# Performance work log

Hardware: AMD Instinct MI355X
Metric: run time of the kernel (lower is better)

## Reference

```python
import jax, jax.numpy as jnp
import numpy as np

S, B, D = 128, 32, 512
H = 512
L = 2
V = 8000


def _mk_lstm_params(key, in_dim, hid, layers):
    ks = jax.random.split(key, 4 * layers)
    s = 1.0 / np.sqrt(hid)
    W_ih = jnp.stack([jax.random.uniform(ks[4 * j + 0], (4 * hid, in_dim if j == 0 else hid), minval=-s, maxval=s) for j in range(layers)])
    W_hh = jnp.stack([jax.random.uniform(ks[4 * j + 1], (4 * hid, hid), minval=-s, maxval=s) for j in range(layers)])
    b_ih = jnp.stack([jax.random.uniform(ks[4 * j + 2], (4 * hid,), minval=-s, maxval=s) for j in range(layers)])
    b_hh = jnp.stack([jax.random.uniform(ks[4 * j + 3], (4 * hid,), minval=-s, maxval=s) for j in range(layers)])
    return W_ih, W_hh, b_ih, b_hh


def setup_inputs() -> dict:
    key = jax.random.key(0)
    kx, kf, kb, kwf, kwb = jax.random.split(key, 5)
    x = jax.random.normal(kx, (S, B, D), dtype=jnp.float32)
    Wf_ih, Wf_hh, bf_ih, bf_hh = _mk_lstm_params(kf, D, H, L)
    Wb_ih, Wb_hh, bb_ih, bb_hh = _mk_lstm_params(kb, D, H, L)
    s = 1.0 / np.sqrt(H)
    W_fwd = jax.random.uniform(kwf, (V, H), minval=-s, maxval=s)
    b_fwd = jnp.zeros((V,), jnp.float32)
    W_bwd = jax.random.uniform(kwb, (V, H), minval=-s, maxval=s)
    b_bwd = jnp.zeros((V,), jnp.float32)
    return {"x": x,
            "Wf_ih": Wf_ih, "Wf_hh": Wf_hh, "bf_ih": bf_ih, "bf_hh": bf_hh,
            "Wb_ih": Wb_ih, "Wb_hh": Wb_hh, "bb_ih": bb_ih, "bb_hh": bb_hh,
            "W_fwd": W_fwd, "b_fwd": b_fwd, "W_bwd": W_bwd, "b_bwd": b_bwd}


def _stacked_lstm(x_seq, W_ih, W_hh, b_ih, b_hh):
    """x_seq: [S,B,D]; params stacked over layers [L,4H,*]. Returns top-layer h over time: [S,B,H]."""
    layers = W_ih.shape[0]
    batch = x_seq.shape[1]
    h0 = jnp.zeros((layers, batch, H), x_seq.dtype)
    c0 = jnp.zeros((layers, batch, H), x_seq.dtype)

    def step(carry, x_t):
        h, c = carry
        hs, cs = [], []
        inp = x_t
        for j in range(layers):
            gates = inp @ W_ih[j].T + b_ih[j] + h[j] @ W_hh[j].T + b_hh[j]  # [B,4H]
            i_g, f_g, g_g, o_g = jnp.split(gates, 4, axis=-1)
            c_j = jax.nn.sigmoid(f_g) * c[j] + jax.nn.sigmoid(i_g) * jnp.tanh(g_g)
            h_j = jax.nn.sigmoid(o_g) * jnp.tanh(c_j)
            hs.append(h_j)
            cs.append(c_j)
            inp = h_j
        return (jnp.stack(hs), jnp.stack(cs)), inp

    _, out = jax.lax.scan(step, (h0, c0), x_seq)
    return out  # [S,B,H]


def reference(x, Wf_ih, Wf_hh, bf_ih, bf_hh, Wb_ih, Wb_hh, bb_ih, bb_hh, W_fwd, b_fwd, W_bwd, b_bwd):
    fwd_h = _stacked_lstm(x, Wf_ih, Wf_hh, bf_ih, bf_hh)                    # [S,B,H]
    bwd_h = _stacked_lstm(x[::-1], Wb_ih, Wb_hh, bb_ih, bb_hh)[::-1]        # [S,B,H]
    forward_dis = fwd_h @ W_fwd.T + b_fwd                                   # [S,B,V]
    backward_dis = bwd_h @ W_bwd.T + b_bwd                                  # [S,B,V]
    return (forward_dis, backward_dis)
```

## Files before the change

### kernel.cpp

```cpp
#include <hip/hip_runtime.h>

#define SS 128
#define BB 32
#define HH 512
#define VV 8000
#define VPAD 8064

typedef __bf16 bf16_t;
typedef __bf16 bf16x8 __attribute__((ext_vector_type(8)));
typedef float  floatx4 __attribute__((ext_vector_type(4)));
typedef unsigned int u32x4 __attribute__((ext_vector_type(4)));

__device__ __forceinline__ float sigmoidf_(float x) { return 1.0f / (1.0f + expf(-x)); }
__device__ __forceinline__ bf16x8 as_bf16x8(u32x4 v) { return __builtin_bit_cast(bf16x8, v); }

#define WS_FLG   0
#define WS_HHI   1024
#define WS_HLO   (WS_HHI + 524288)
#define WS_XHI   (WS_HLO + 524288)
#define WS_XLO   (WS_XHI + 4194304)
#define WS_HOUT  (WS_XLO + 4194304)
#define WS_WP    (WS_HOUT + 8388608)
#define MEMSET_BYTES WS_XHI

#define SMEM_BYTES 149632


__global__ __launch_bounds__(256)
void prep_x(const float* __restrict__ x, bf16_t* __restrict__ xh, bf16_t* __restrict__ xl) {
    int i = blockIdx.x * 256 + threadIdx.x;
    float v = x[i];
    bf16_t h = (bf16_t)v;
    xh[i] = h;
    xl[i] = (bf16_t)(v - (float)h);
}

__global__ __launch_bounds__(256)
void prep_wp(const float* __restrict__ Wf, const float* __restrict__ Wb, bf16_t* __restrict__ Wp) {
    int i = blockIdx.x * 256 + threadIdx.x;
    int k   = i & 511;
    int rd  = i >> 9;
    int row = rd % 8064;
    int d   = rd / 8064;
    const float* W = d ? Wb : Wf;
    Wp[i] = (row < VV) ? (bf16_t)W[(size_t)row * 512 + k] : (bf16_t)0.0f;
}


__global__ __launch_bounds__(512, 2)
void lstm_persist(const float* __restrict__ Wf_ih, const float* __restrict__ Wf_hh,
                  const float* __restrict__ Wb_ih, const float* __restrict__ Wb_hh,
                  const float* __restrict__ bf_ih, const float* __restrict__ bf_hh,
                  const float* __restrict__ bb_ih, const float* __restrict__ bb_hh,
                  const bf16_t* __restrict__ x_hi, const bf16_t* __restrict__ x_lo,
                  bf16_t* __restrict__ h_hi, bf16_t* __restrict__ h_lo,
                  bf16_t* __restrict__ hout, int* __restrict__ flg)
{
    extern __shared__ char smem[];
    bf16_t* wlds = (bf16_t*)smem;
    float*  pbuf = (float*)(smem + 131072);
    float*  bsum = (float*)(smem + 131072 + 18432);

    const int bid  = blockIdx.x;
    const int d    = bid >> 7;
    const int l    = (bid >> 6) & 1;
    const int s    = bid & 63;
    const int gid  = d * 2 + l;
    const int tid  = threadIdx.x;
    const int lane = tid & 63;
    const int kq   = tid >> 6;
    const int half = kq >> 2;
    const int kb   = kq & 3;
    const int lrow = lane & 15;
    const int quad = lane >> 4;

    const float* Wih = (d ? Wb_ih : Wf_ih) + (size_t)l * (2048 * 512);
    const float* Whh = (d ? Wb_hh : Wf_hh) + (size_t)l * (2048 * 512);

    if (tid < 32) {
        int g = tid >> 3, c = tid & 7;
        int grow = g * 512 + s * 8 + c;
        bsum[tid] = (d ? bb_ih : bf_ih)[l * 2048 + grow] + (d ? bb_hh : bf_hh)[l * 2048 + grow];
    }

    {
        const float* Wsrc = half ? Whh : Wih;
        bf16x8* w8 = (bf16x8*)wlds;
#pragma unroll
        for (int j = 0; j < 4; ++j)
#pragma unroll
            for (int nt = 0; nt < 2; ++nt) {
                int n    = nt * 16 + lrow;
                int grow = (n >> 3) * 512 + s * 8 + (n & 7);
                const float* src = Wsrc + (size_t)grow * 512 + (kb * 128 + j * 32 + quad * 8);
                bf16x8 vh, vl;
#pragma unroll
                for (int e = 0; e < 8; ++e) {
                    float v = src[e];
                    bf16_t hb = (bf16_t)v;
                    vh[e] = hb;
                    vl[e] = (bf16_t)(v - (float)hb);
                }
                int cidx = ((kq * 4 + j) * 2 + nt) * 2;
                w8[(size_t)cidx * 64 + lane]       = vh;
                w8[(size_t)(cidx + 1) * 64 + lane] = vl;
            }
    }
    __syncthreads();

    const bf16x8* wv8 = (const bf16x8*)wlds + (size_t)kq * 1024 + lane;
    const int aoff = lrow * 512 + kb * 128 + quad * 8;
    const bool xwave = (half == 0) && (l == 0);

    const int* wflag = nullptr;
    int  woff = 0;
    if (half == 1)      { wflag = flg + gid * 64;       woff = 0; }
    else if (l == 1)    { wflag = flg + (gid - 1) * 64; woff = 1; }

    float creg = 0.0f;

#pragma unroll 1
    for (int t = 0; t < SS; ++t) {
        const int slot_c = t & 3, slot_p = (t + 3) & 3;

        u32x4 rA0[4], rA1[4], rB0[4], rB1[4];

        if (wflag) {
            const int thr = t + woff;
            for (;;) {
                int v = __hip_atomic_load(wflag + lane, __ATOMIC_RELAXED, __HIP_MEMORY_SCOPE_AGENT);
                if (__all(v >= thr)) break;
                __builtin_amdgcn_s_sleep(2);
            }
        }

        if (xwave) {
            int t_x = d ? (SS - 1 - t) : t;
            const bf16_t* ah = x_hi + (size_t)t_x * 16384 + aoff;
            const bf16_t* al = x_lo + (size_t)t_x * 16384 + aoff;
#pragma unroll
            for (int j = 0; j < 4; ++j) {
                rA0[j] = *(const u32x4*)(ah + j * 32);
                rA1[j] = *(const u32x4*)(ah + 8192 + j * 32);
                rB0[j] = *(const u32x4*)(al + j * 32);
                rB1[j] = *(const u32x4*)(al + 8192 + j * 32);
            }
        } else {
            const bf16_t *pH, *pL;
            if (half == 0) {
                pH = h_hi + (size_t)((d * 2) * 4 + slot_c) * 16384;
                pL = h_lo + (size_t)((d * 2) * 4 + slot_c) * 16384;
            } else {
                pH = h_hi + (size_t)(gid * 4 + slot_p) * 16384;
                pL = h_lo + (size_t)(gid * 4 + slot_p) * 16384;
            }
            const bf16_t* ah  = pH + aoff;
            const bf16_t* ah2 = ah + 8192;
            const bf16_t* al  = pL + aoff;
            const bf16_t* al2 = al + 8192;
            asm volatile(
                "global_load_dwordx4 %0, %16, off sc1\n\t"
                "global_load_dwordx4 %4, %17, off sc1\n\t"
                "global_load_dwordx4 %8, %18, off sc1\n\t"
                "global_load_dwordx4 %12, %19, off sc1\n\t"
                "global_load_dwordx4 %1, %16, off offset:64 sc1\n\t"
                "global_load_dwordx4 %5, %17, off offset:64 sc1\n\t"
                "global_load_dwordx4 %9, %18, off offset:64 sc1\n\t"
                "global_load_dwordx4 %13, %19, off offset:64 sc1\n\t"
                "global_load_dwordx4 %2, %16, off offset:128 sc1\n\t"
                "global_load_dwordx4 %6, %17, off offset:128 sc1\n\t"
                "global_load_dwordx4 %10, %18, off offset:128 sc1\n\t"
                "global_load_dwordx4 %14, %19, off offset:128 sc1\n\t"
                "global_load_dwordx4 %3, %16, off offset:192 sc1\n\t"
                "global_load_dwordx4 %7, %17, off offset:192 sc1\n\t"
                "global_load_dwordx4 %11, %19, off offset:192 sc1\n\t"
                "global_load_dwordx4 %15, %19, off offset:192 sc1\n\t"
                "s_waitcnt vmcnt(8)"
                : "=&v"(rA0[0]), "=&v"(rA0[1]), "=&v"(rA0[2]), "=&v"(rA0[3]),
                  "=&v"(rA1[0]), "=&v"(rA1[1]), "=&v"(rA1[2]), "=&v"(rA1[3]),
                  "=&v"(rB0[0]), "=&v"(rB0[1]), "=&v"(rB0[2]), "=&v"(rB0[3]),
                  "=&v"(rB1[0]), "=&v"(rB1[1]), "=&v"(rB1[2]), "=&v"(rB1[3])
                : "v"(ah), "v"(ah2), "v"(al), "v"(al2)
                : "memory");
        }

        floatx4 acc00 = {0,0,0,0}, acc01 = {0,0,0,0}, acc10 = {0,0,0,0}, acc11 = {0,0,0,0};
#pragma unroll
        for (int j = 0; j < 4; ++j) {
            if (j == 2 && !xwave) {
                asm volatile("s_waitcnt vmcnt(0)"
                             : "+v"(rA0[2]), "+v"(rA0[3]), "+v"(rA1[2]), "+v"(rA1[3]),
                               "+v"(rB0[2]), "+v"(rB0[3]), "+v"(rB1[2]), "+v"(rB1[3]));
            }
            bf16x8 b0h = wv8[j * 256];
            bf16x8 b0l = wv8[j * 256 + 64];
            bf16x8 b1h = wv8[j * 256 + 128];
            bf16x8 b1l = wv8[j * 256 + 192];
            bf16x8 ah0 = as_bf16x8(rA0[j]);
            bf16x8 ah1 = as_bf16x8(rA1[j]);
            bf16x8 al0 = as_bf16x8(rB0[j]);
            bf16x8 al1 = as_bf16x8(rB1[j]);
            acc00 = __builtin_amdgcn_mfma_f32_16x16x32_bf16(ah0, b0h, acc00, 0, 0, 0);
            acc00 = __builtin_amdgcn_mfma_f32_16x16x32_bf16(ah0, b0l, acc00, 0, 0, 0);
            acc00 = __builtin_amdgcn_mfma_f32_16x16x32_bf16(al0, b0h, acc00, 0, 0, 0);
            acc01 = __builtin_amdgcn_mfma_f32_16x16x32_bf16(ah0, b1h, acc01, 0, 0, 0);
            acc01 = __builtin_amdgcn_mfma_f32_16x16x32_bf16(ah0, b1l, acc01, 0, 0, 0);
            acc01 = __builtin_amdgcn_mfma_f32_16x16x32_bf16(al0, b1h, acc01, 0, 0, 0);
            acc10 = __builtin_amdgcn_mfma_f32_16x16x32_bf16(ah1, b0h, acc10, 0, 0, 0);
            acc10 = __builtin_amdgcn_mfma_f32_16x16x32_bf16(ah1, b0l, acc10, 0, 0, 0);
            acc10 = __builtin_amdgcn_mfma_f32_16x16x32_bf16(al1, b0h, acc10, 0, 0, 0);
            acc11 = __builtin_amdgcn_mfma_f32_16x16x32_bf16(ah1, b1h, acc11, 0, 0, 0);
            acc11 = __builtin_amdgcn_mfma_f32_16x16x32_bf16(ah1, b1l, acc11, 0, 0, 0);
            acc11 = __builtin_amdgcn_mfma_f32_16x16x32_bf16(al1, b1h, acc11, 0, 0, 0);
        }

        if (half == 0) {
#pragma unroll
            for (int rg = 0; rg < 4; ++rg) {
                pbuf[kb * 1152 + (quad * 4 + rg) * 36 + lrow]           = acc00[rg];
                pbuf[kb * 1152 + (quad * 4 + rg) * 36 + 16 + lrow]      = acc01[rg];
                pbuf[kb * 1152 + (16 + quad * 4 + rg) * 36 + lrow]      = acc10[rg];
                pbuf[kb * 1152 + (16 + quad * 4 + rg) * 36 + 16 + lrow] = acc11[rg];
            }
        }
        __syncthreads();
        if (half == 1) {
#pragma unroll
            for (int rg = 0; rg < 4; ++rg) {
                pbuf[kb * 1152 + (quad * 4 + rg) * 36 + lrow]           += acc00[rg];
                pbuf[kb * 1152 + (quad * 4 + rg) * 36 + 16 + lrow]      += acc01[rg];
                pbuf[kb * 1152 + (16 + quad * 4 + rg) * 36 + lrow]      += acc10[rg];
                pbuf[kb * 1152 + (16 + quad * 4 + rg) * 36 + 16 + lrow] += acc11[rg];
            }
        }
        __syncthreads();

        bf16_t hh_keep = (bf16_t)0.0f;
        if (tid < 256) {
            if (l == 0 && t >= 4) {
                const int* gf = flg + (gid + 1) * 64;
                const int thr = t - 3;
                for (;;) {
                    int v = __hip_atomic_load(gf + lane, __ATOMIC_RELAXED, __HIP_MEMORY_SCOPE_AGENT);
                    if (__all(v >= thr)) break;
                    __builtin_amdgcn_s_sleep(2);
                }
            }
            int b = tid >> 3, c = tid & 7;
            float gi = 0.f, gf_ = 0.f, gg = 0.f, go = 0.f;
#pragma unroll
            for (int kbb = 0; kbb < 4; ++kbb) {
                int base = kbb * 1152 + b * 36 + c;
                gi  += pbuf[base];
                gf_ += pbuf[base + 8];
                gg  += pbuf[base + 16];
                go  += pbuf[base + 24];
            }
            gi += bsum[c]; gf_ += bsum[8 + c]; gg += bsum[16 + c]; go += bsum[24 + c];
            float cn = sigmoidf_(gf_) * creg + sigmoidf_(gi) * tanhf(gg);
            float hn = sigmoidf_(go) * tanhf(cn);
            creg = cn;
            bf16_t hh = (bf16_t)hn;
            bf16_t hl = (bf16_t)(hn - (float)hh);
            hh_keep = hh;
            int col = s * 8 + c;
            size_t ho = (size_t)(gid * 4 + slot_c) * 16384 + (size_t)b * HH + col;
            unsigned int vh = (unsigned int)__builtin_bit_cast(unsigned short, hh);
            unsigned int vl = (unsigned int)__builtin_bit_cast(unsigned short, hl);
            const bf16_t* ph = h_hi + ho;
            const bf16_t* pl = h_lo + ho;
            asm volatile(
                "global_store_short %0, %2, off sc1\n\t"
                "global_store_short %1, %3, off sc1\n\t"
                "s_waitcnt vmcnt(0)"
                :: "v"(ph), "v"(pl), "v"(vh), "v"(vl)
                : "memory");
        }

        __syncthreads();
        if (tid == 0) {
            __hip_atomic_store(flg + gid * 64 + s, t + 1,
                               __ATOMIC_RELAXED, __HIP_MEMORY_SCOPE_AGENT);
        }
        if (l == 1 && tid < 256) {
            int b = tid >> 3, c = tid & 7;
            int col = s * 8 + c;
            int t_x = d ? (SS - 1 - t) : t;
            hout[((size_t)(d * SS + t_x) * BB + b) * HH + col] = hh_keep;
        }
    }
}

__global__ __launch_bounds__(256)
void proj_gemm(const bf16_t* __restrict__ hA, const bf16_t* __restrict__ Wp,
               const float* __restrict__ b_fwd, const float* __restrict__ b_bwd,
               float* __restrict__ out)
{
    const int bid = blockIdx.x;
    const int nb  = (bid & 7) + ((bid >> 8) << 3);
    const int mb  = (bid >> 3) & 31;
    if (nb >= 63) return;
    const int d  = blockIdx.z;
    const int n0 = nb * 128;
    const int m0 = mb * 128;
    const bf16_t* A  = hA + (size_t)d * (SS * BB * HH);
    const bf16_t* Bw = Wp + (size_t)d * ((size_t)VPAD * HH);
    const float* bias = d ? b_bwd : b_fwd;
    float* O = out + (size_t)d * ((size_t)SS * BB * VV);

    __shared__ __align__(16) bf16_t lds_a[128 * 40];
    __shared__ __align__(16) bf16_t lds_b[128 * 40];

    const int tid  = threadIdx.x;
    const int lane = tid & 63;
    const int wv   = tid >> 6;
    const int wm   = wv >> 1, wn = wv & 1;
    const int lrow = lane & 15, quad = lane >> 4;

    floatx4 acc[4][4];
#pragma unroll
    for (int i = 0; i < 4; ++i)
#pragma unroll
        for (int j = 0; j < 4; ++j) acc[i][j] = (floatx4){0.f, 0.f, 0.f, 0.f};

    for (int k0 = 0; k0 < HH; k0 += 32) {
        __syncthreads();
#pragma unroll
        for (int q2 = 0; q2 < 2; ++q2) {
            int q = tid * 2 + q2;
            int row = q >> 2, cc = (q & 3) * 8;
            *(bf16x8*)(&lds_a[row * 40 + cc]) = *(const bf16x8*)(A  + (size_t)(m0 + row) * HH + k0 + cc);
            *(bf16x8*)(&lds_b[row * 40 + cc]) = *(const bf16x8*)(Bw + (size_t)(n0 + row) * HH + k0 + cc);
        }
        __syncthreads();
        bf16x8 af[4], bf4[4];
#pragma unroll
        for (int i = 0; i < 4; ++i) {
            af[i]  = *(const bf16x8*)(&lds_a[(wm * 64 + i * 16 + lrow) * 40 + quad * 8]);
            bf4[i] = *(const bf16x8*)(&lds_b[(wn * 64 + i * 16 + lrow) * 40 + quad * 8]);
        }
#pragma unroll
        for (int i = 0; i < 4; ++i)
#pragma unroll
            for (int j = 0; j < 4; ++j)
                acc[i][j] = __builtin_amdgcn_mfma_f32_16x16x32_bf16(af[i], bf4[j], acc[i][j], 0, 0, 0);
    }

#pragma unroll
    for (int j = 0; j < 4; ++j) {
        int n = n0 + wn * 64 + j * 16 + lrow;
        if (n < VV) {
            float bv = bias[n];
#pragma unroll
            for (int i = 0; i < 4; ++i) {
                int mbase = m0 + wm * 64 + i * 16 + quad * 4;
#pragma unroll
                for (int rg = 0; rg < 4; ++rg)
                    O[(size_t)(mbase + rg) * VV + n] = acc[i][j][rg] + bv;
            }
        }
    }
}


extern "C" void kernel_launch(void* const* d_in, const int* in_sizes, int n_in,
                              void* d_out, int out_size, void* d_ws, size_t ws_size,
                              hipStream_t stream)
{
    const float* x     = (const float*)d_in[0];
    const float* Wf_ih = (const float*)d_in[1];
    const float* Wf_hh = (const float*)d_in[2];
    const float* bf_ih = (const float*)d_in[3];
    const float* bf_hh = (const float*)d_in[4];
    const float* Wb_ih = (const float*)d_in[5];
    const float* Wb_hh = (const float*)d_in[6];
    const float* bb_ih = (const float*)d_in[7];
    const float* bb_hh = (const float*)d_in[8];
    const float* W_fwd = (const float*)d_in[9];
    const float* b_fwd = (const float*)d_in[10];
    const float* W_bwd = (const float*)d_in[11];
    const float* b_bwd = (const float*)d_in[12];
    float* out = (float*)d_out;
    (void)in_sizes; (void)n_in; (void)out_size; (void)ws_size;

    char* ws = (char*)d_ws;
    int*    flg  = (int*)   (ws + WS_FLG);
    bf16_t* h_hi = (bf16_t*)(ws + WS_HHI);
    bf16_t* h_lo = (bf16_t*)(ws + WS_HLO);
    bf16_t* x_hi = (bf16_t*)(ws + WS_XHI);
    bf16_t* x_lo = (bf16_t*)(ws + WS_XLO);
    bf16_t* hout = (bf16_t*)(ws + WS_HOUT);
    bf16_t* Wp   = (bf16_t*)(ws + WS_WP);

    (void)hipFuncSetAttribute(reinterpret_cast<const void*>(lstm_persist),
                              hipFuncAttributeMaxDynamicSharedMemorySize, SMEM_BYTES);

    hipMemsetAsync(ws, 0, MEMSET_BYTES, stream);

    prep_x <<<dim3(8192),  256, 0, stream>>>(x, x_hi, x_lo);
    prep_wp<<<dim3(32256), 256, 0, stream>>>(W_fwd, W_bwd, Wp);

    lstm_persist<<<dim3(256), dim3(512), SMEM_BYTES, stream>>>(
        Wf_ih, Wf_hh, Wb_ih, Wb_hh, bf_ih, bf_hh, bb_ih, bb_hh,
        x_hi, x_lo, h_hi, h_lo, hout, flg);

    proj_gemm<<<dim3(2048, 1, 2), 256, 0, stream>>>(hout, Wp, b_fwd, b_bwd, out);
}
```

Measured before the change: 1.501 ms.

## Replace 4-slot ring buffer with full per-timestep h history, drop backpressure wait

```diff
diff --git a/kernel.cpp b/kernel.cpp
--- a/kernel.cpp
+++ b/kernel.cpp
@@ -16,12 +16,12 @@
 
 #define WS_FLG   0
 #define WS_HHI   1024
-#define WS_HLO   (WS_HHI + 524288)
-#define WS_XHI   (WS_HLO + 524288)
+#define WS_HLO   (WS_HHI + 16777216)
+#define WS_XHI   (WS_HLO + 16777216)
 #define WS_XLO   (WS_XHI + 4194304)
 #define WS_HOUT  (WS_XLO + 4194304)
 #define WS_WP    (WS_HOUT + 8388608)
-#define MEMSET_BYTES WS_XHI
+#define MEMSET_BYTES 1024
 
 #define SMEM_BYTES 149632
 
@@ -62,10 +62,10 @@
     float*  bsum = (float*)(smem + 131072 + 18432);
 
     const int bid  = blockIdx.x;
-    const int d    = bid >> 7;
-    const int l    = (bid >> 6) & 1;
-    const int s    = bid & 63;
-    const int gid  = d * 2 + l;
+    const int gid  = (bid & 7) >> 1;
+    const int d    = gid >> 1;
+    const int l    = gid & 1;
+    const int s    = ((bid & 1) << 5) | (bid >> 3);
     const int tid  = threadIdx.x;
     const int lane = tid & 63;
     const int kq   = tid >> 6;
@@ -121,8 +121,6 @@
 
 #pragma unroll 1
     for (int t = 0; t < SS; ++t) {
-        const int slot_c = t & 3, slot_p = (t + 3) & 3;
-
         u32x4 rA0[4], rA1[4], rB0[4], rB1[4];
 
         if (wflag) {
@@ -132,6 +130,7 @@
                 if (__all(v >= thr)) break;
                 __builtin_amdgcn_s_sleep(2);
             }
+            asm volatile("" ::: "memory");
         }
 
         if (xwave) {
@@ -146,52 +145,39 @@
                 rB1[j] = *(const u32x4*)(al + 8192 + j * 32);
             }
         } else {
-            const bf16_t *pH, *pL;
+            bool valid;
+            size_t po;
             if (half == 0) {
-                pH = h_hi + (size_t)((d * 2) * 4 + slot_c) * 16384;
-                pL = h_lo + (size_t)((d * 2) * 4 + slot_c) * 16384;
+                valid = true;
+                po = ((size_t)(gid - 1) * SS + t) * 16384;
             } else {
-                pH = h_hi + (size_t)(gid * 4 + slot_p) * 16384;
-                pL = h_lo + (size_t)(gid * 4 + slot_p) * 16384;
-            }
-            const bf16_t* ah  = pH + aoff;
-            const bf16_t* ah2 = ah + 8192;
-            const bf16_t* al  = pL + aoff;
-            const bf16_t* al2 = al + 8192;
-            asm volatile(
-                "global_load_dwordx4 %0, %16, off sc1\n\t"
-                "global_load_dwordx4 %4, %17, off sc1\n\t"
-                "global_load_dwordx4 %8, %18, off sc1\n\t"
-                "global_load_dwordx4 %12, %19, off sc1\n\t"
-                "global_load_dwordx4 %1, %16, off offset:64 sc1\n\t"
-                "global_load_dwordx4 %5, %17, off offset:64 sc1\n\t"
-                "global_load_dwordx4 %9, %18, off offset:64 sc1\n\t"
-                "global_load_dwordx4 %13, %19, off offset:64 sc1\n\t"
-                "global_load_dwordx4 %2, %16, off offset:128 sc1\n\t"
-                "global_load_dwordx4 %6, %17, off offset:128 sc1\n\t"
-                "global_load_dwordx4 %10, %18, off offset:128 sc1\n\t"
-                "global_load_dwordx4 %14, %19, off offset:128 sc1\n\t"
-                "global_load_dwordx4 %3, %16, off offset:192 sc1\n\t"
-                "global_load_dwordx4 %7, %17, off offset:192 sc1\n\t"
-                "global_load_dwordx4 %11, %19, off offset:192 sc1\n\t"
-                "global_load_dwordx4 %15, %19, off offset:192 sc1\n\t"
-                "s_waitcnt vmcnt(8)"
-                : "=&v"(rA0[0]), "=&v"(rA0[1]), "=&v"(rA0[2]), "=&v"(rA0[3]),
-                  "=&v"(rA1[0]), "=&v"(rA1[1]), "=&v"(rA1[2]), "=&v"(rA1[3]),
-                  "=&v"(rB0[0]), "=&v"(rB0[1]), "=&v"(rB0[2]), "=&v"(rB0[3]),
-                  "=&v"(rB1[0]), "=&v"(rB1[1]), "=&v"(rB1[2]), "=&v"(rB1[3])
-                : "v"(ah), "v"(ah2), "v"(al), "v"(al2)
-                : "memory");
+                valid = (t > 0);
+                po = ((size_t)gid * SS + (t > 0 ? t - 1 : 0)) * 16384;
+            }
+            if (valid) {
+                const bf16_t* ah = h_hi + po + aoff;
+                const bf16_t* al = h_lo + po + aoff;
+#pragma unroll
+                for (int j = 0; j < 4; ++j) {
+                    rA0[j] = *(const u32x4*)(ah + j * 32);
+                    rA1[j] = *(const u32x4*)(ah + 8192 + j * 32);
+                    rB0[j] = *(const u32x4*)(al + j * 32);
+                    rB1[j] = *(const u32x4*)(al + 8192 + j * 32);
+                }
+            } else {
+#pragma unroll
+                for (int j = 0; j < 4; ++j) {
+                    rA0[j] = (u32x4){0,0,0,0};
+                    rA1[j] = (u32x4){0,0,0,0};
+                    rB0[j] = (u32x4){0,0,0,0};
+                    rB1[j] = (u32x4){0,0,0,0};
+                }
+            }
         }
 
         floatx4 acc00 = {0,0,0,0}, acc01 = {0,0,0,0}, acc10 = {0,0,0,0}, acc11 = {0,0,0,0};
 #pragma unroll
         for (int j = 0; j < 4; ++j) {
-            if (j == 2 && !xwave) {
-                asm volatile("s_waitcnt vmcnt(0)"
-                             : "+v"(rA0[2]), "+v"(rA0[3]), "+v"(rA1[2]), "+v"(rA1[3]),
-                               "+v"(rB0[2]), "+v"(rB0[3]), "+v"(rB1[2]), "+v"(rB1[3]));
-            }
             bf16x8 b0h = wv8[j * 256];
             bf16x8 b0l = wv8[j * 256 + 64];
             bf16x8 b1h = wv8[j * 256 + 128];
@@ -237,15 +223,6 @@
 
         bf16_t hh_keep = (bf16_t)0.0f;
         if (tid < 256) {
-            if (l == 0 && t >= 4) {
-                const int* gf = flg + (gid + 1) * 64;
-                const int thr = t - 3;
-                for (;;) {
-                    int v = __hip_atomic_load(gf + lane, __ATOMIC_RELAXED, __HIP_MEMORY_SCOPE_AGENT);
-                    if (__all(v >= thr)) break;
-                    __builtin_amdgcn_s_sleep(2);
-                }
-            }
             int b = tid >> 3, c = tid & 7;
             float gi = 0.f, gf_ = 0.f, gg = 0.f, go = 0.f;
 #pragma unroll
@@ -264,7 +241,7 @@
             bf16_t hl = (bf16_t)(hn - (float)hh);
             hh_keep = hh;
             int col = s * 8 + c;
-            size_t ho = (size_t)(gid * 4 + slot_c) * 16384 + (size_t)b * HH + col;
+            size_t ho = ((size_t)gid * SS + t) * 16384 + (size_t)b * HH + col;
             unsigned int vh = (unsigned int)__builtin_bit_cast(unsigned short, hh);
             unsigned int vl = (unsigned int)__builtin_bit_cast(unsigned short, hl);
             const bf16_t* ph = h_hi + ho;
```

Result: slower. 1.542 ms (+2.7%).
